# Performance work log

Hardware: AMD Instinct MI355X
Metric: run time of the kernel (lower is better)

## Reference

```python
import jax, jax.numpy as jnp
import numpy as np

B, C_IN, C_OUT, N, K = 16, 128, 128, 4096, 16


def setup_inputs() -> dict:
    key = jax.random.key(0)
    k1, k2, k3, k4 = jax.random.split(key, 4)
    x = jax.random.normal(k1, (B, C_IN, N, 1), dtype=jnp.float32)
    edge_index = jax.random.randint(k2, (2, B, N, K), 0, N, dtype=jnp.int32)
    # 1x1 conv weight of BasicConv([C_IN, C_OUT], 'relu', None, bias=False)
    W = jax.random.normal(k3, (C_OUT, C_IN), dtype=jnp.float32) * (1.0 / np.sqrt(C_IN))
    # module bias param, initialized to zeros; use random here to exercise the add
    bias = jax.random.normal(k4, (1, C_OUT, 1, 1), dtype=jnp.float32) * 0.01
    return {"x": x, "edge_index": edge_index, "W": W, "bias": bias}


def reference(x, edge_index, W, bias):
    b, _, n, _ = x.shape
    # BasicConv: 1x1 conv (no bias) + ReLU
    h = jax.nn.relu(jnp.einsum('oi,binu->bonu', W, x))  # [B, C_out, N, 1]
    h2 = h[..., 0]                                       # [B, C_out, N]
    # add_self_loops: append self index along neighbor dim
    self_idx = jnp.broadcast_to(jnp.arange(n, dtype=edge_index.dtype)[None, None, :, None],
                                (2, b, n, 1))
    ei = jnp.concatenate([edge_index, self_idx], axis=-1)  # [2, B, N, K+1]
    idx = ei[0]                                            # [B, N, K+1]
    deg = ei.shape[-1]
    norm = 1.0 / deg
    # batched_index_select: gather neighbor features -> [B, C_out, N, K+1]
    x_j = jax.vmap(lambda hb, ib: hb[:, ib])(h2, idx)
    aggr = (x_j * norm).sum(axis=-1, keepdims=True)        # [B, C_out, N, 1]
    return aggr + bias
```

## Files before the change

### kernel.cpp

```cpp
#include <hip/hip_runtime.h>

#define B_    16
#define CIN_  128
#define COUT_ 128
#define N_    4096
#define K_    16

typedef __attribute__((ext_vector_type(8))) short bf16x8;
typedef __attribute__((ext_vector_type(4))) float f32x4;
typedef __attribute__((ext_vector_type(4))) int   i32x4;
typedef __attribute__((ext_vector_type(2))) float f32x2;

__device__ inline unsigned short f2bf(float f) {
  unsigned u = __float_as_uint(f);
  u += 0x7fffu + ((u >> 16) & 1u);
  return (unsigned short)(u >> 16);
}

__global__ __launch_bounds__(256) void gemm_relu_k(
    const float* __restrict__ x, const float* __restrict__ W,
    unsigned short* __restrict__ h) {
  __shared__ unsigned short Wl[128 * 136];
  const int tid = threadIdx.x;
  const int b   = blockIdx.x >> 5;
  const int n0  = (blockIdx.x & 31) * 128;

#pragma unroll
  for (int r = 0; r < 16; ++r) {
    int id = tid + 256 * r;
    int co = id >> 5;
    int cq = id & 31;
    float4 v = reinterpret_cast<const float4*>(W)[id];
    unsigned p0 = (unsigned)f2bf(v.x) | ((unsigned)f2bf(v.y) << 16);
    unsigned p1 = (unsigned)f2bf(v.z) | ((unsigned)f2bf(v.w) << 16);
    *reinterpret_cast<uint2*>(&Wl[co * 136 + 4 * cq]) = make_uint2(p0, p1);
  }
  __syncthreads();

  const int lane = tid & 63;
  const int w    = tid >> 6;
  const int m    = lane & 15;
  const int quad = lane >> 4;

  const float* xb = x + (size_t)b * CIN_ * N_ + n0 + 32 * w + m;
  bf16x8 a[2][4];
#pragma unroll
  for (int p = 0; p < 2; ++p) {
#pragma unroll
    for (int s = 0; s < 4; ++s) {
#pragma unroll
      for (int j = 0; j < 8; ++j) {
        int ci = 32 * s + 8 * quad + j;
        a[p][s][j] = (short)f2bf(xb[(size_t)ci * N_ + 16 * p]);
      }
    }
  }

  unsigned short* hb = h + (size_t)b * N_ * COUT_;
  const int rbase = n0 + 32 * w + 4 * quad;
#pragma unroll
  for (int t = 0; t < 8; ++t) {
    f32x4 c0 = {0.f, 0.f, 0.f, 0.f}, c1 = c0;
#pragma unroll
    for (int s = 0; s < 4; ++s) {
      bf16x8 bf = *reinterpret_cast<const bf16x8*>(
          &Wl[(16 * t + m) * 136 + 32 * s + 8 * quad]);
      c0 = __builtin_amdgcn_mfma_f32_16x16x32_bf16(a[0][s], bf, c0, 0, 0, 0);
      c1 = __builtin_amdgcn_mfma_f32_16x16x32_bf16(a[1][s], bf, c1, 0, 0, 0);
    }
    int co = 16 * t + m;
#pragma unroll
    for (int r = 0; r < 4; ++r) {
      float v0 = c0[r] > 0.f ? c0[r] : 0.f;
      float v1 = c1[r] > 0.f ? c1[r] : 0.f;
      hb[(size_t)(rbase + r) * COUT_ + co]      = f2bf(v0);
      hb[(size_t)(rbase + 16 + r) * COUT_ + co] = f2bf(v1);
    }
  }
}

__global__ __launch_bounds__(256) void aggr_k(
    const unsigned short* __restrict__ h, const int* __restrict__ ei,
    const float* __restrict__ bias, float* __restrict__ out, int phase) {
  __shared__ int idx_t[K_ * 32];
  const int tid = threadIdx.x;
  const int b   = 8 * phase + (blockIdx.x & 7);
  const int n0  = (blockIdx.x >> 3) * 32;

  if (tid < 128) {
    int n  = tid >> 2;
    int kq = tid & 3;
    i32x4 v = __builtin_nontemporal_load(
        reinterpret_cast<const i32x4*>(ei + ((size_t)b * N_ + n0 + n) * K_) + kq);
    idx_t[(4 * kq + 0) * 32 + n] = v.x;
    idx_t[(4 * kq + 1) * 32 + n] = v.y;
    idx_t[(4 * kq + 2) * 32 + n] = v.z;
    idx_t[(4 * kq + 3) * 32 + n] = v.w;
  }
  __syncthreads();

  const int q = tid & 15;
  const int g = tid >> 4;
  const unsigned short* hb = h + (size_t)b * N_ * COUT_;

  float acc[2][8];
#pragma unroll
  for (int j = 0; j < 2; ++j) {
    uint4 v = *reinterpret_cast<const uint4*>(
        hb + (size_t)(n0 + 2 * g + j) * COUT_ + 8 * q);
    acc[j][0] = __uint_as_float(v.x << 16);
    acc[j][1] = __uint_as_float(v.x & 0xffff0000u);
    acc[j][2] = __uint_as_float(v.y << 16);
    acc[j][3] = __uint_as_float(v.y & 0xffff0000u);
    acc[j][4] = __uint_as_float(v.z << 16);
    acc[j][5] = __uint_as_float(v.z & 0xffff0000u);
    acc[j][6] = __uint_as_float(v.w << 16);
    acc[j][7] = __uint_as_float(v.w & 0xffff0000u);
  }
#pragma unroll 4
  for (int k = 0; k < K_; ++k) {
    int2 jj = *reinterpret_cast<const int2*>(&idx_t[k * 32 + 2 * g]);
#pragma unroll
    for (int j = 0; j < 2; ++j) {
      int node = (j == 0) ? jj.x : jj.y;
      uint4 v = *reinterpret_cast<const uint4*>(
          hb + (size_t)node * COUT_ + 8 * q);
      acc[j][0] += __uint_as_float(v.x << 16);
      acc[j][1] += __uint_as_float(v.x & 0xffff0000u);
      acc[j][2] += __uint_as_float(v.y << 16);
      acc[j][3] += __uint_as_float(v.y & 0xffff0000u);
      acc[j][4] += __uint_as_float(v.z << 16);
      acc[j][5] += __uint_as_float(v.z & 0xffff0000u);
      acc[j][6] += __uint_as_float(v.w << 16);
      acc[j][7] += __uint_as_float(v.w & 0xffff0000u);
    }
  }

  const float norm = 1.0f / 17.0f;
  const float4 bv0 = *reinterpret_cast<const float4*>(bias + 8 * q);
  const float4 bv1 = *reinterpret_cast<const float4*>(bias + 8 * q + 4);
  float* ob = out + (size_t)b * COUT_ * N_ + n0 + 2 * g;
#pragma unroll
  for (int c = 0; c < 8; ++c) {
    int co = 8 * q + c;
    float bb = (c < 4) ? ((c == 0) ? bv0.x : (c == 1) ? bv0.y : (c == 2) ? bv0.z : bv0.w)
                       : ((c == 4) ? bv1.x : (c == 5) ? bv1.y : (c == 6) ? bv1.z : bv1.w);
    f32x2 r;
    r.x = acc[0][c] * norm + bb;
    r.y = acc[1][c] * norm + bb;
    __builtin_nontemporal_store(r, reinterpret_cast<f32x2*>(ob + (size_t)co * N_));
  }
}

extern "C" void kernel_launch(void* const* d_in, const int* in_sizes, int n_in,
                              void* d_out, int out_size, void* d_ws, size_t ws_size,
                              hipStream_t stream) {
  const float* x    = (const float*)d_in[0];
  const int*   ei   = (const int*)d_in[1];
  const float* W    = (const float*)d_in[2];
  const float* bias = (const float*)d_in[3];
  float* out = (float*)d_out;
  unsigned short* h = (unsigned short*)d_ws;

  gemm_relu_k<<<dim3(B_ * N_ / 128), 256, 0, stream>>>(x, W, h);
  aggr_k<<<dim3(8 * (N_ / 32)), 256, 0, stream>>>(h, ei, bias, out, 0);
  aggr_k<<<dim3(8 * (N_ / 32)), 256, 0, stream>>>(h, ei, bias, out, 1);
}
```

Baseline: 130.2 us.

## Halve GEMM tile per block, remap batches to XCDs, merge aggregation launches

```diff
diff --git a/kernel.cpp b/kernel.cpp
--- a/kernel.cpp
+++ b/kernel.cpp
@@ -22,8 +22,9 @@
     unsigned short* __restrict__ h) {
   __shared__ unsigned short Wl[128 * 136];
   const int tid = threadIdx.x;
-  const int b   = blockIdx.x >> 5;
-  const int n0  = (blockIdx.x & 31) * 128;
+  const int l   = blockIdx.x;
+  const int b   = ((l & 7) << 1) | ((l >> 3) >> 6);
+  const int n0  = ((l >> 3) & 63) * 64;
 
 #pragma unroll
   for (int r = 0; r < 16; ++r) {
@@ -42,50 +43,46 @@
   const int m    = lane & 15;
   const int quad = lane >> 4;
 
-  const float* xb = x + (size_t)b * CIN_ * N_ + n0 + 32 * w + m;
-  bf16x8 a[2][4];
+  const float* xb = x + (size_t)b * CIN_ * N_ + n0 + 16 * w + m;
+  bf16x8 a[4];
 #pragma unroll
-  for (int p = 0; p < 2; ++p) {
+  for (int s = 0; s < 4; ++s) {
 #pragma unroll
-    for (int s = 0; s < 4; ++s) {
-#pragma unroll
-      for (int j = 0; j < 8; ++j) {
-        int ci = 32 * s + 8 * quad + j;
-        a[p][s][j] = (short)f2bf(xb[(size_t)ci * N_ + 16 * p]);
-      }
+    for (int j = 0; j < 8; ++j) {
+      int ci = 32 * s + 8 * quad + j;
+      a[s][j] = (short)f2bf(xb[(size_t)ci * N_]);
     }
   }
 
+  const int rbase = n0 + 16 * w + 4 * quad;
   unsigned short* hb = h + (size_t)b * N_ * COUT_;
-  const int rbase = n0 + 32 * w + 4 * quad;
 #pragma unroll
   for (int t = 0; t < 8; ++t) {
-    f32x4 c0 = {0.f, 0.f, 0.f, 0.f}, c1 = c0;
+    f32x4 c = {0.f, 0.f, 0.f, 0.f};
 #pragma unroll
     for (int s = 0; s < 4; ++s) {
       bf16x8 bf = *reinterpret_cast<const bf16x8*>(
           &Wl[(16 * t + m) * 136 + 32 * s + 8 * quad]);
-      c0 = __builtin_amdgcn_mfma_f32_16x16x32_bf16(a[0][s], bf, c0, 0, 0, 0);
-      c1 = __builtin_amdgcn_mfma_f32_16x16x32_bf16(a[1][s], bf, c1, 0, 0, 0);
+      c = __builtin_amdgcn_mfma_f32_16x16x32_bf16(a[s], bf, c, 0, 0, 0);
     }
     int co = 16 * t + m;
 #pragma unroll
     for (int r = 0; r < 4; ++r) {
-      float v0 = c0[r] > 0.f ? c0[r] : 0.f;
-      float v1 = c1[r] > 0.f ? c1[r] : 0.f;
-      hb[(size_t)(rbase + r) * COUT_ + co]      = f2bf(v0);
-      hb[(size_t)(rbase + 16 + r) * COUT_ + co] = f2bf(v1);
+      float v = c[r] > 0.f ? c[r] : 0.f;
+      hb[(size_t)(rbase + r) * COUT_ + co] = f2bf(v);
     }
   }
 }
 
 __global__ __launch_bounds__(256) void aggr_k(
     const unsigned short* __restrict__ h, const int* __restrict__ ei,
-    const float* __restrict__ bias, float* __restrict__ out, int phase) {
+    const float* __restrict__ bias, float* __restrict__ out) {
   __shared__ int idx_t[K_ * 32];
-  const int tid = threadIdx.x;
-  const int b   = 8 * phase + (blockIdx.x & 7);
-  const int n0  = (blockIdx.x >> 3) * 32;
+  const int tid  = threadIdx.x;
+  const int l    = blockIdx.x;
+  const int rest = l >> 3;
+  const int b    = ((l & 7) << 1) | (rest >> 7);
+  const int n0   = (rest & 127) * 32;
 
   if (tid < 128) {
     int n  = tid >> 2;
@@ -162,7 +159,6 @@
   float* out = (float*)d_out;
   unsigned short* h = (unsigned short*)d_ws;
 
-  gemm_relu_k<<<dim3(B_ * N_ / 128), 256, 0, stream>>>(x, W, h);
-  aggr_k<<<dim3(8 * (N_ / 32)), 256, 0, stream>>>(h, ei, bias, out, 0);
-  aggr_k<<<dim3(8 * (N_ / 32)), 256, 0, stream>>>(h, ei, bias, out, 1);
+  gemm_relu_k<<<dim3(B_ * N_ / 64), 256, 0, stream>>>(x, W, h);
+  aggr_k<<<dim3(B_ * N_ / 32), 256, 0, stream>>>(h, ei, bias, out);
 }
```

Measured after the change: 150.7 us. 1.16x slower.
